# Performance work log

Measured on AMD Instinct MI355X. Metric: run time of the kernel, lower is better.

## Reference

```python
import jax, jax.numpy as jnp
import numpy as np

# Fixed problem sizes (uniform frames so the irregular loop vectorizes)
S = 32            # number of frames (sequences)
N = 128           # pedestrians per frame
H = 64            # pool_h_dim (lstm hidden dim)
G = 8             # grid_size
NS = 2.0          # neighbourhood_size
OUT = 64          # pool_out_dim
EPS = 1e-5        # BatchNorm1d eps


def setup_inputs() -> dict:
    key = jax.random.key(0)
    k1, k2, k3 = jax.random.split(key, 3)
    hidden_states = jax.random.normal(k1, (S * N, H), jnp.float32)
    # positions in [0, 4): neighbourhood of size 2 captures many neighbours
    all_pos = jax.random.uniform(k2, (S * N, 2), jnp.float32) * 4.0
    W = jax.random.normal(k3, (G * G * H, OUT), jnp.float32) * 0.02
    b = jnp.zeros((OUT,), jnp.float32)
    gamma = jnp.ones((OUT,), jnp.float32)
    beta = jnp.zeros((OUT,), jnp.float32)
    starts = jnp.arange(S, dtype=jnp.int32) * N
    seq_start_end = jnp.stack([starts, starts + N], axis=1)
    return {"hidden_states": hidden_states, "all_pos": all_pos, "W": W,
            "b": b, "gamma": gamma, "beta": beta,
            "seq_start_end": seq_start_end}


def _pool_one_frame(hs, ps):
    # hs: [N, H] hidden states, ps: [N, 2] positions of one frame.
    # Pair (i, j): bbox around ped i, contribution from ped j's hidden state.
    xi, yi = ps[:, 0][:, None], ps[:, 1][:, None]   # bbox owner i -> rows
    xj, yj = ps[:, 0][None, :], ps[:, 1][None, :]   # neighbour j -> cols
    half = NS / 2
    tlx, tly = xi - half, yi + half                 # top-left of bbox(i)
    brx, bry = xi + half, yi - half                 # bottom-right of bbox(i)
    gx = jnp.floor((xj - tlx) / NS * G)
    gy = jnp.floor((tly - yj) / NS * G)
    grid = (gx + G * gy).astype(jnp.int32) + 1      # +1: slot 0 is dump bin
    # out-of-bbox or self -> masked to bin 0
    mask = ((xj <= tlx) | (yj >= tly) | (xj >= brx) | (yj <= bry)
            | jnp.eye(N, dtype=bool))
    grid = grid + (jnp.arange(N, dtype=jnp.int32) * (G * G))[:, None]
    grid = jnp.where(mask, 0, grid)                 # [N, N]
    vals = jnp.broadcast_to(hs[None, :, :], (N, N, H)).reshape(N * N, H)
    pooled = jax.ops.segment_sum(vals, grid.reshape(-1),
                                 num_segments=N * G * G + 1)[1:]
    return pooled.reshape(N, G * G * H)


def reference(hidden_states, all_pos, W, b, gamma, beta, seq_start_end):
    h = hidden_states.reshape(S, N, H)
    p = all_pos.reshape(S, N, 2)
    pool_h = jax.vmap(_pool_one_frame)(h, p).reshape(S * N, G * G * H)
    x = pool_h @ W + b
    # BatchNorm1d in training mode: biased batch statistics
    mean = jnp.mean(x, axis=0)
    var = jnp.mean((x - mean) ** 2, axis=0)
    x = (x - mean) / jnp.sqrt(var + EPS) * gamma + beta
    return jax.nn.relu(x)
```

## Files before the change

kernel.cpp:

```cpp
#include <hip/hip_runtime.h>
#include <math.h>

#define NFRAMES 32
#define NPED    128
#define HDIM    64
#define KDIM    4096
#define OUTD    64
#define EPSV    1e-5f
#define NBLK    512
#define MROW    16
#define PROW    2056
#define HROW    136

typedef __attribute__((ext_vector_type(8))) short  short8;
typedef __attribute__((ext_vector_type(4))) float  floatx4;

static __device__ __forceinline__ unsigned short f2bf(float f) {
    union { float f; unsigned u; } v; v.f = f;
    unsigned r = v.u + 0x7fffu + ((v.u >> 16) & 1u);
    return (unsigned short)(r >> 16);
}

static __device__ __forceinline__ int kperm(int k) {
    return (k & 0xC0F) | ((k >> 2) & 0x0F0) | ((k & 0x030) << 4);
}

__global__ void k_wt(const float* __restrict__ W, unsigned short* __restrict__ Wt,
                     float* __restrict__ x) {
    __shared__ float T[64 * 65];
    const int t  = threadIdx.x;
    const int k0 = blockIdx.x * 64;
    {
        float4 z = {0.f, 0.f, 0.f, 0.f};
        ((float4*)x)[blockIdx.x * 1024 + t]       = z;
        ((float4*)x)[blockIdx.x * 1024 + 512 + t] = z;
    }
    #pragma unroll
    for (int it = 0; it < 8; ++it) {
        int idx = it * 512 + t;
        int kl = idx >> 6, o = idx & 63;
        T[kl * 65 + o] = W[(size_t)(k0 + kl) * OUTD + o];
    }
    __syncthreads();
    {
        int o  = t & 63;
        int kl = (t >> 6) * 8;
        unsigned pk[4];
        #pragma unroll
        for (int e = 0; e < 4; ++e) {
            pk[e] = (unsigned)f2bf(T[(kl + 2 * e) * 65 + o]) |
                    ((unsigned)f2bf(T[(kl + 2 * e + 1) * 65 + o]) << 16);
        }
        int klog = kperm(k0 + kl);
        int wn   = o >> 4;
        int q    = klog >> 10;
        int s    = (klog >> 5) & 31;
        int quad = (klog >> 3) & 3;
        int ln   = quad * 16 + (o & 15);
        unsigned short* dst = Wt + ((size_t)((wn * 4 + q) * 32 + s) * 64 + ln) * 8;
        *(uint4*)dst = (uint4){pk[0], pk[1], pk[2], pk[3]};
    }
}

__global__ __launch_bounds__(512, 4) void k_fused(
    const float* __restrict__ hs, const float* __restrict__ pos,
    const unsigned short* __restrict__ Wt, float* __restrict__ x)
{
    __shared__ char SM[MROW * PROW * 2 + 2048 + 1024];
    unsigned short* P    = (unsigned short*)SM;
    unsigned short* HsT  = (unsigned short*)SM;
    float*          red  = (float*)SM;
    unsigned char*  CT   = (unsigned char*)(SM + MROW * PROW * 2);
    float*          posL = (float*)(SM + MROW * PROW * 2 + 2048);

    const int tid   = threadIdx.x;
    const int bid   = blockIdx.x;
    const int f     = bid >> 4;
    const int chunk = (bid >> 1) & 7;
    const int kh    = bid & 1;
    const int lane  = tid & 63;
    const int w     = tid >> 6;
    const int m     = lane & 15;
    const int quad  = lane >> 4;

    if (tid < 256) posL[tid] = pos[f * (NPED * 2) + tid];
    const float* hsF = hs + f * (NPED * HDIM);
    #pragma unroll
    for (int it = 0; it < 4; ++it) {
        int g = it * 512 + tid;
        float4 v = ((const float4*)hsF)[g];
        int j  = g >> 4;
        int h0 = (g & 15) * 4;
        HsT[(h0 + 0) * HROW + j] = f2bf(v.x);
        HsT[(h0 + 1) * HROW + j] = f2bf(v.y);
        HsT[(h0 + 2) * HROW + j] = f2bf(v.z);
        HsT[(h0 + 3) * HROW + j] = f2bf(v.w);
    }
    __syncthreads();

    const int i0 = chunk * 16;
    #pragma unroll
    for (int it = 0; it < 4; ++it) {
        int idx = it * 512 + tid;
        int i = idx >> 7, j = idx & 127;
        float xi = posL[(i0 + i) * 2], yi = posL[(i0 + i) * 2 + 1];
        float xj = posL[j * 2],        yj = posL[j * 2 + 1];
        float tlx = xi - 1.0f, tly = yi + 1.0f;
        bool valid = (xj > tlx) & (yj < tly) & (xj < xi + 1.0f) &
                     (yj > yi - 1.0f) & (j != i0 + i);
        int gx = (int)floorf((xj - tlx) * 4.0f);
        int gy = (int)floorf((tly - yj) * 4.0f);
        int c  = gx + 8 * gy;
        CT[i * NPED + j] = (valid && (unsigned)c < 64u) ? (unsigned char)c : 255;
    }

    short8 Af[4][4];
    #pragma unroll
    for (int ht = 0; ht < 4; ++ht)
        #pragma unroll
        for (int kt = 0; kt < 4; ++kt)
            Af[ht][kt] = *(const short8*)&HsT[(ht * 16 + m) * HROW + kt * 32 + quad * 8];
    __syncthreads();

    #pragma unroll
    for (int r = 0; r < 2; ++r) {
        const int i = w * 2 + r;
        const unsigned char* ctRow = CT + i * NPED;
        floatx4 pa[4][2];
        #pragma unroll
        for (int ht = 0; ht < 4; ++ht)
            #pragma unroll
            for (int c2 = 0; c2 < 2; ++c2) pa[ht][c2] = (floatx4){0.f, 0.f, 0.f, 0.f};
        #pragma unroll
        for (int kt = 0; kt < 4; ++kt) {
            unsigned long long cb = *(const unsigned long long*)(ctRow + kt * 32 + quad * 8);
            unsigned lo = (unsigned)cb, hi = (unsigned)(cb >> 32);
            int b0 = (int)(lo & 255u), b1 = (int)((lo >> 8) & 255u);
            int b2 = (int)((lo >> 16) & 255u), b3 = (int)(lo >> 24);
            int b4 = (int)(hi & 255u), b5 = (int)((hi >> 8) & 255u);
            int b6 = (int)((hi >> 16) & 255u), b7 = (int)(hi >> 24);
            #pragma unroll
            for (int c2 = 0; c2 < 2; ++c2) {
                const int tgt = (kh * 2 + c2) * 16 + m;
                union { int iv[4]; short8 sv; } B;
                B.iv[0] = (b0 == tgt ? 0x00003F80 : 0) | (b1 == tgt ? 0x3F800000 : 0);
                B.iv[1] = (b2 == tgt ? 0x00003F80 : 0) | (b3 == tgt ? 0x3F800000 : 0);
                B.iv[2] = (b4 == tgt ? 0x00003F80 : 0) | (b5 == tgt ? 0x3F800000 : 0);
                B.iv[3] = (b6 == tgt ? 0x00003F80 : 0) | (b7 == tgt ? 0x3F800000 : 0);
                #pragma unroll
                for (int ht = 0; ht < 4; ++ht)
                    pa[ht][c2] = __builtin_amdgcn_mfma_f32_16x16x32_bf16(Af[ht][kt], B.sv, pa[ht][c2], 0, 0, 0);
            }
        }
        #pragma unroll
        for (int c2 = 0; c2 < 2; ++c2)
            #pragma unroll
            for (int ht = 0; ht < 4; ++ht) {
                union { floatx4 fv; unsigned uv[4]; } U; U.fv = pa[ht][c2];
                uint2 pv;
                pv.x = __builtin_amdgcn_perm(U.uv[1], U.uv[0], 0x07060302u);
                pv.y = __builtin_amdgcn_perm(U.uv[3], U.uv[2], 0x07060302u);
                *reinterpret_cast<uint2*>(&P[i * PROW + c2 * 1024 + ht * 256 + m * 16 + quad * 4]) = pv;
            }
    }
    __syncthreads();

    const int wn = w & 3;
    const int wq = w >> 2;
    const int q  = kh * 2 + wq;
    floatx4 acc[4];
    #pragma unroll
    for (int u = 0; u < 4; ++u) acc[u] = (floatx4){0.f, 0.f, 0.f, 0.f};
    const unsigned short* Prow = P + m * PROW + wq * 1024;
    const unsigned short* wB   = Wt + ((size_t)(wn * 4 + q) * 32 * 64 + lane) * 8;
    #pragma unroll 8
    for (int s = 0; s < 32; ++s) {
        short8 a = *(const short8*)(Prow + s * 32 + quad * 8);
        short8 b = *(const short8*)(wB + s * 512);
        acc[s & 3] = __builtin_amdgcn_mfma_f32_16x16x32_bf16(a, b, acc[s & 3], 0, 0, 0);
    }
    floatx4 accf = (acc[0] + acc[1]) + (acc[2] + acc[3]);
    __syncthreads();

    if (wq == 1) *(floatx4*)(red + (wn * 64 + lane) * 4) = accf;
    __syncthreads();
    if (wq == 0) {
        accf += *(const floatx4*)(red + (wn * 64 + lane) * 4);
        const int ibase = f * NPED + chunk * 16;
        #pragma unroll
        for (int r = 0; r < 4; ++r) {
            int row = quad * 4 + r;
            atomicAdd(&x[(size_t)(ibase + row) * OUTD + wn * 16 + m], accf[r]);
        }
    }
}

__global__ __launch_bounds__(512) void k_apply(
    const float* __restrict__ x, const float* __restrict__ gamma,
    const float* __restrict__ beta, float* __restrict__ out) {
    __shared__ float sW1[8][OUTD], sW2[8][OUTD];
    __shared__ float muL[OUTD], isL[OUTD];
    const int t = threadIdx.x, lane = t & 63, w = t >> 6;
    float4 s1v = {0.f, 0.f, 0.f, 0.f}, s2v = {0.f, 0.f, 0.f, 0.f};
    const float4* x4 = (const float4*)x;
    #pragma unroll 8
    for (int r = 0; r < 128; ++r) {
        float4 v = x4[r * 512 + t];
        s1v.x += v.x; s1v.y += v.y; s1v.z += v.z; s1v.w += v.w;
        s2v.x += v.x * v.x; s2v.y += v.y * v.y; s2v.z += v.z * v.z; s2v.w += v.w * v.w;
    }
    #pragma unroll
    for (int d = 16; d <= 32; d <<= 1) {
        s1v.x += __shfl_xor(s1v.x, d); s1v.y += __shfl_xor(s1v.y, d);
        s1v.z += __shfl_xor(s1v.z, d); s1v.w += __shfl_xor(s1v.w, d);
        s2v.x += __shfl_xor(s2v.x, d); s2v.y += __shfl_xor(s2v.y, d);
        s2v.z += __shfl_xor(s2v.z, d); s2v.w += __shfl_xor(s2v.w, d);
    }
    if (lane < 16) {
        sW1[w][lane * 4 + 0] = s1v.x; sW1[w][lane * 4 + 1] = s1v.y;
        sW1[w][lane * 4 + 2] = s1v.z; sW1[w][lane * 4 + 3] = s1v.w;
        sW2[w][lane * 4 + 0] = s2v.x; sW2[w][lane * 4 + 1] = s2v.y;
        sW2[w][lane * 4 + 2] = s2v.z; sW2[w][lane * 4 + 3] = s2v.w;
    }
    __syncthreads();
    if (t < OUTD) {
        float s1 = 0.f, s2 = 0.f;
        #pragma unroll
        for (int ww = 0; ww < 8; ++ww) { s1 += sW1[ww][t]; s2 += sW2[ww][t]; }
        const float inv_n = 1.0f / (float)(NFRAMES * NPED);
        float mu  = s1 * inv_n;
        float var = s2 * inv_n - mu * mu;
        muL[t] = mu;
        isL[t] = rsqrtf(var + EPSV);
    }
    __syncthreads();
    #pragma unroll
    for (int i = 0; i < 4; ++i) {
        int g  = blockIdx.x * 2048 + i * 512 + t;
        int o0 = (g & 15) * 4;
        float4 xv = ((const float4*)x)[g];
        float4 r;
        r.x = (xv.x - muL[o0 + 0]) * isL[o0 + 0] * gamma[o0 + 0] + beta[o0 + 0];
        r.y = (xv.y - muL[o0 + 1]) * isL[o0 + 1] * gamma[o0 + 1] + beta[o0 + 1];
        r.z = (xv.z - muL[o0 + 2]) * isL[o0 + 2] * gamma[o0 + 2] + beta[o0 + 2];
        r.w = (xv.w - muL[o0 + 3]) * isL[o0 + 3] * gamma[o0 + 3] + beta[o0 + 3];
        r.x = r.x > 0.f ? r.x : 0.f;
        r.y = r.y > 0.f ? r.y : 0.f;
        r.z = r.z > 0.f ? r.z : 0.f;
        r.w = r.w > 0.f ? r.w : 0.f;
        ((float4*)out)[g] = r;
    }
}

extern "C" void kernel_launch(void* const* d_in, const int* in_sizes, int n_in,
                              void* d_out, int out_size, void* d_ws, size_t ws_size,
                              hipStream_t stream) {
    const float* hs    = (const float*)d_in[0];
    const float* pos   = (const float*)d_in[1];
    const float* W     = (const float*)d_in[2];
    const float* gamma = (const float*)d_in[4];
    const float* beta  = (const float*)d_in[5];

    char* ws = (char*)d_ws;
    unsigned short* Wt = (unsigned short*)ws;
    float* x = (float*)(ws + (512 << 10));

    k_wt   <<<KDIM / 64, 512, 0, stream>>>(W, Wt, x);
    k_fused<<<NBLK, 512, 0, stream>>>(hs, pos, Wt, x);
    k_apply<<<32, 512, 0, stream>>>(x, gamma, beta, (float*)d_out);
}
```

Baseline: 94.72 us.

## Replace atomic K-split reduction with per-quarter partial buffers summed in BN kernel

The fused kernel no longer does a shared-memory cross-wave reduction followed by atomicAdd into a zeroed x buffer. Each K-quarter instead writes its partial result with plain stores into its own slice of a 4x buffer, and k_apply sums the four partials while computing BatchNorm statistics and again when normalising. This removes the x zeroing pass, two barriers and the atomics, and the positions are now read straight from global memory instead of being staged in LDS. In exchange k_apply reads four times as much data and runs on half as many blocks, and k_wt gains a dummy read of hs that looks meant to prefetch it into cache.

Result: slower. 124.5 us (+31.4%).

```diff
diff --git a/kernel.cpp b/kernel.cpp
--- a/kernel.cpp
+++ b/kernel.cpp
@@ -11,6 +11,7 @@
 #define MROW    16
 #define PROW    2056
 #define HROW    136
+#define XQN     (NFRAMES * NPED * OUTD)
 
 typedef __attribute__((ext_vector_type(8))) short  short8;
 typedef __attribute__((ext_vector_type(4))) float  floatx4;
@@ -26,20 +27,21 @@
 }
 
 __global__ void k_wt(const float* __restrict__ W, unsigned short* __restrict__ Wt,
-                     float* __restrict__ x) {
+                     const float* __restrict__ hs) {
     __shared__ float T[64 * 65];
     const int t  = threadIdx.x;
     const int k0 = blockIdx.x * 64;
-    {
-        float4 z = {0.f, 0.f, 0.f, 0.f};
-        ((float4*)x)[blockIdx.x * 1024 + t]       = z;
-        ((float4*)x)[blockIdx.x * 1024 + 512 + t] = z;
-    }
     #pragma unroll
     for (int it = 0; it < 8; ++it) {
         int idx = it * 512 + t;
         int kl = idx >> 6, o = idx & 63;
         T[kl * 65 + o] = W[(size_t)(k0 + kl) * OUTD + o];
+    }
+    {
+        const float4* h4 = (const float4*)hs + blockIdx.x * 1024;
+        float4 a = h4[t], b = h4[512 + t];
+        float s = (a.x + a.y + a.z + a.w) + (b.x + b.y + b.z + b.w);
+        asm volatile("" :: "v"(s));
     }
     __syncthreads();
     {
@@ -64,14 +66,12 @@
 
 __global__ __launch_bounds__(512, 4) void k_fused(
     const float* __restrict__ hs, const float* __restrict__ pos,
-    const unsigned short* __restrict__ Wt, float* __restrict__ x)
+    const unsigned short* __restrict__ Wt, float* __restrict__ xq)
 {
-    __shared__ char SM[MROW * PROW * 2 + 2048 + 1024];
+    __shared__ char SM[MROW * PROW * 2 + 2048];
     unsigned short* P    = (unsigned short*)SM;
     unsigned short* HsT  = (unsigned short*)SM;
-    float*          red  = (float*)SM;
     unsigned char*  CT   = (unsigned char*)(SM + MROW * PROW * 2);
-    float*          posL = (float*)(SM + MROW * PROW * 2 + 2048);
 
     const int tid   = threadIdx.x;
     const int bid   = blockIdx.x;
@@ -83,7 +83,6 @@
     const int m     = lane & 15;
     const int quad  = lane >> 4;
 
-    if (tid < 256) posL[tid] = pos[f * (NPED * 2) + tid];
     const float* hsF = hs + f * (NPED * HDIM);
     #pragma unroll
     for (int it = 0; it < 4; ++it) {
@@ -96,23 +95,23 @@
         HsT[(h0 + 2) * HROW + j] = f2bf(v.z);
         HsT[(h0 + 3) * HROW + j] = f2bf(v.w);
     }
-    __syncthreads();
-
+    const float2* pf = (const float2*)pos + f * NPED;
     const int i0 = chunk * 16;
     #pragma unroll
     for (int it = 0; it < 4; ++it) {
         int idx = it * 512 + tid;
         int i = idx >> 7, j = idx & 127;
-        float xi = posL[(i0 + i) * 2], yi = posL[(i0 + i) * 2 + 1];
-        float xj = posL[j * 2],        yj = posL[j * 2 + 1];
-        float tlx = xi - 1.0f, tly = yi + 1.0f;
-        bool valid = (xj > tlx) & (yj < tly) & (xj < xi + 1.0f) &
-                     (yj > yi - 1.0f) & (j != i0 + i);
-        int gx = (int)floorf((xj - tlx) * 4.0f);
-        int gy = (int)floorf((tly - yj) * 4.0f);
+        float2 pi = pf[i0 + i];
+        float2 pj = pf[j];
+        float tlx = pi.x - 1.0f, tly = pi.y + 1.0f;
+        bool valid = (pj.x > tlx) & (pj.y < tly) & (pj.x < pi.x + 1.0f) &
+                     (pj.y > pi.y - 1.0f) & (j != i0 + i);
+        int gx = (int)floorf((pj.x - tlx) * 4.0f);
+        int gy = (int)floorf((tly - pj.y) * 4.0f);
         int c  = gx + 8 * gy;
         CT[i * NPED + j] = (valid && (unsigned)c < 64u) ? (unsigned char)c : 255;
     }
+    __syncthreads();
 
     short8 Af[4][4];
     #pragma unroll
@@ -180,34 +179,34 @@
         acc[s & 3] = __builtin_amdgcn_mfma_f32_16x16x32_bf16(a, b, acc[s & 3], 0, 0, 0);
     }
     floatx4 accf = (acc[0] + acc[1]) + (acc[2] + acc[3]);
-    __syncthreads();
-
-    if (wq == 1) *(floatx4*)(red + (wn * 64 + lane) * 4) = accf;
-    __syncthreads();
-    if (wq == 0) {
-        accf += *(const floatx4*)(red + (wn * 64 + lane) * 4);
-        const int ibase = f * NPED + chunk * 16;
-        #pragma unroll
-        for (int r = 0; r < 4; ++r) {
-            int row = quad * 4 + r;
-            atomicAdd(&x[(size_t)(ibase + row) * OUTD + wn * 16 + m], accf[r]);
-        }
+
+    float* xqp = xq + (size_t)q * XQN;
+    const int ibase = f * NPED + chunk * 16;
+    #pragma unroll
+    for (int r = 0; r < 4; ++r) {
+        int row = quad * 4 + r;
+        xqp[(size_t)(ibase + row) * OUTD + wn * 16 + m] = accf[r];
     }
 }
 
 __global__ __launch_bounds__(512) void k_apply(
-    const float* __restrict__ x, const float* __restrict__ gamma,
+    const float* __restrict__ xq, const float* __restrict__ gamma,
     const float* __restrict__ beta, float* __restrict__ out) {
     __shared__ float sW1[8][OUTD], sW2[8][OUTD];
     __shared__ float muL[OUTD], isL[OUTD];
     const int t = threadIdx.x, lane = t & 63, w = t >> 6;
+    const float4* x4 = (const float4*)xq;
     float4 s1v = {0.f, 0.f, 0.f, 0.f}, s2v = {0.f, 0.f, 0.f, 0.f};
-    const float4* x4 = (const float4*)x;
-    #pragma unroll 8
+    #pragma unroll 4
     for (int r = 0; r < 128; ++r) {
-        float4 v = x4[r * 512 + t];
-        s1v.x += v.x; s1v.y += v.y; s1v.z += v.z; s1v.w += v.w;
-        s2v.x += v.x * v.x; s2v.y += v.y * v.y; s2v.z += v.z * v.z; s2v.w += v.w * v.w;
+        int g = r * 512 + t;
+        float4 a = x4[g], b = x4[65536 + g], c = x4[131072 + g], d = x4[196608 + g];
+        float vx = (a.x + b.x) + (c.x + d.x);
+        float vy = (a.y + b.y) + (c.y + d.y);
+        float vz = (a.z + b.z) + (c.z + d.z);
+        float vw = (a.w + b.w) + (c.w + d.w);
+        s1v.x += vx; s1v.y += vy; s1v.z += vz; s1v.w += vw;
+        s2v.x += vx * vx; s2v.y += vy * vy; s2v.z += vz * vz; s2v.w += vw * vw;
     }
     #pragma unroll
     for (int d = 16; d <= 32; d <<= 1) {
@@ -235,15 +234,15 @@
     }
     __syncthreads();
     #pragma unroll
-    for (int i = 0; i < 4; ++i) {
-        int g  = blockIdx.x * 2048 + i * 512 + t;
+    for (int i = 0; i < 8; ++i) {
+        int g  = blockIdx.x * 4096 + i * 512 + t;
         int o0 = (g & 15) * 4;
-        float4 xv = ((const float4*)x)[g];
+        float4 a = x4[g], b = x4[65536 + g], c = x4[131072 + g], d = x4[196608 + g];
         float4 r;
-        r.x = (xv.x - muL[o0 + 0]) * isL[o0 + 0] * gamma[o0 + 0] + beta[o0 + 0];
-        r.y = (xv.y - muL[o0 + 1]) * isL[o0 + 1] * gamma[o0 + 1] + beta[o0 + 1];
-        r.z = (xv.z - muL[o0 + 2]) * isL[o0 + 2] * gamma[o0 + 2] + beta[o0 + 2];
-        r.w = (xv.w - muL[o0 + 3]) * isL[o0 + 3] * gamma[o0 + 3] + beta[o0 + 3];
+        r.x = ((a.x + b.x) + (c.x + d.x) - muL[o0 + 0]) * isL[o0 + 0] * gamma[o0 + 0] + beta[o0 + 0];
+        r.y = ((a.y + b.y) + (c.y + d.y) - muL[o0 + 1]) * isL[o0 + 1] * gamma[o0 + 1] + beta[o0 + 1];
+        r.z = ((a.z + b.z) + (c.z + d.z) - muL[o0 + 2]) * isL[o0 + 2] * gamma[o0 + 2] + beta[o0 + 2];
+        r.w = ((a.w + b.w) + (c.w + d.w) - muL[o0 + 3]) * isL[o0 + 3] * gamma[o0 + 3] + beta[o0 + 3];
         r.x = r.x > 0.f ? r.x : 0.f;
         r.y = r.y > 0.f ? r.y : 0.f;
         r.z = r.z > 0.f ? r.z : 0.f;
@@ -263,9 +262,9 @@
 
     char* ws = (char*)d_ws;
     unsigned short* Wt = (unsigned short*)ws;
-    float* x = (float*)(ws + (512 << 10));
-
-    k_wt   <<<KDIM / 64, 512, 0, stream>>>(W, Wt, x);
-    k_fused<<<NBLK, 512, 0, stream>>>(hs, pos, Wt, x);
-    k_apply<<<32, 512, 0, stream>>>(x, gamma, beta, (float*)d_out);
-}
+    float* xq = (float*)(ws + (512 << 10));
+
+    k_wt   <<<KDIM / 64, 512, 0, stream>>>(W, Wt, hs);
+    k_fused<<<NBLK, 512, 0, stream>>>(hs, pos, Wt, xq);
+    k_apply<<<16, 512, 0, stream>>>(xq, gamma, beta, (float*)d_out);
+}
```
